# Optimization experiments

Hardware: AMD Instinct MI355X
Metric: run time of the kernel (lower is better)

## Reference

```python
import jax, jax.numpy as jnp
import numpy as np

N_BINS = 10
EPS = 1e-07


def setup_inputs() -> dict:
    key = jax.random.key(0)
    k1, k2 = jax.random.split(key)
    N, C = 8_000_000, 10
    logits = jax.random.uniform(k1, (N, C), dtype=jnp.float32)
    labels = jax.random.randint(k2, (N,), 0, C, dtype=jnp.int64)
    return {"logits": logits, "labels": labels}


def reference(logits, labels):
    # Faithful to torch forward: softmaxes = logits - 1e-7, then max/argmax over classes.
    boundaries = jnp.linspace(0.0, 1.0, N_BINS + 1, dtype=jnp.float32)
    sm = logits - EPS
    confidences = jnp.max(sm, axis=1)          # [N]
    predictions = jnp.argmax(sm, axis=1)       # [N]
    accuracies = (predictions == labels).astype(jnp.float32)

    # in_bin = conf > bin_lower & conf <= bin_upper  <=>  searchsorted(left) - 1
    # (boundaries[i-1] < conf <= boundaries[i] -> bin i-1)
    bin_idx = jnp.searchsorted(boundaries, confidences, side="left") - 1
    valid = (bin_idx >= 0) & (bin_idx < N_BINS)
    seg = jnp.where(valid, bin_idx, N_BINS)    # out-of-range -> overflow segment

    counts = jax.ops.segment_sum(jnp.ones_like(confidences), seg,
                                 num_segments=N_BINS + 1)[:N_BINS]
    correct = jax.ops.segment_sum(accuracies, seg,
                                  num_segments=N_BINS + 1)[:N_BINS]
    # accuracy_in_bin if prop_in_bin > 0 else 0
    return jnp.where(counts > 0, correct / jnp.maximum(counts, 1.0), 0.0)
```

## Files before the change

kernel.cpp:

```cpp
#include <hip/hip_runtime.h>

#define N_BINS 10
#define EPS 1e-7f

typedef unsigned int uint;


__global__ void zero_ws_kernel(uint* ws) {
    if (threadIdx.x < 2 * N_BINS) ws[threadIdx.x] = 0u;
}

__device__ __forceinline__ void process_row(const float v[10], int label,
                                            uint& c8, uint& k8, uint& c9, uint& k9,
                                            uint* scount, uint* scorrect) {
    float m = v[0] - EPS;
    int am = 0;
#pragma unroll
    for (int j = 1; j < 10; ++j) {
        float s = v[j] - EPS;
        if (s > m) { m = s; am = j; }
    }
    int acc = (am == label) ? 1 : 0;

    int idx = 0;
#pragma unroll
    for (int j = 0; j <= 10; ++j) {
        idx += ((0.1f * (float)j) < m) ? 1 : 0;
    }
    int bin = idx - 1;

    if (bin == 9)      { c9++; k9 += acc; }
    else if (bin == 8) { c8++; k8 += acc; }
    else if (bin >= 0 && bin < 8) {
        atomicAdd(&scount[bin], 1u);
        if (acc) atomicAdd(&scorrect[bin], 1u);
    }
}

__global__ void __launch_bounds__(512)
hist_kernel(const float* __restrict__ logits, const int* __restrict__ labels,
            uint* __restrict__ ws, int npairs, int n_rows) {
    __shared__ uint scount[N_BINS];
    __shared__ uint scorrect[N_BINS];
    if (threadIdx.x < N_BINS) { scount[threadIdx.x] = 0u; scorrect[threadIdx.x] = 0u; }
    __syncthreads();

    uint c8 = 0, k8 = 0, c9 = 0, k9 = 0;

    const int stride = gridDim.x * blockDim.x;
    const int tid0   = blockIdx.x * blockDim.x + threadIdx.x;

    for (int p = tid0; p < npairs; p += stride) {
        const float4* lp = reinterpret_cast<const float4*>(logits) + (size_t)p * 5;
        float4 q0 = lp[0], q1 = lp[1], q2 = lp[2], q3 = lp[3], q4 = lp[4];
        int2 lab = reinterpret_cast<const int2*>(labels)[p];

        float a[10] = { q0.x, q0.y, q0.z, q0.w, q1.x, q1.y, q1.z, q1.w, q2.x, q2.y };
        float b[10] = { q2.z, q2.w, q3.x, q3.y, q3.z, q3.w, q4.x, q4.y, q4.z, q4.w };

        process_row(a, lab.x, c8, k8, c9, k9, scount, scorrect);
        process_row(b, lab.y, c8, k8, c9, k9, scount, scorrect);
    }

    if ((n_rows & 1) && tid0 == 0) {
        const float* rp = logits + (size_t)(n_rows - 1) * 10;
        float t[10];
#pragma unroll
        for (int j = 0; j < 10; ++j) t[j] = rp[j];
        process_row(t, labels[n_rows - 1], c8, k8, c9, k9, scount, scorrect);
    }

#pragma unroll
    for (int off = 32; off > 0; off >>= 1) {
        c8 += __shfl_down(c8, off);
        k8 += __shfl_down(k8, off);
        c9 += __shfl_down(c9, off);
        k9 += __shfl_down(k9, off);
    }
    if ((threadIdx.x & 63) == 0) {
        atomicAdd(&scount[8], c8);
        atomicAdd(&scorrect[8], k8);
        atomicAdd(&scount[9], c9);
        atomicAdd(&scorrect[9], k9);
    }
    __syncthreads();

    if (threadIdx.x < N_BINS) {
        atomicAdd(&ws[threadIdx.x], scount[threadIdx.x]);
        atomicAdd(&ws[N_BINS + threadIdx.x], scorrect[threadIdx.x]);
    }
}

__global__ void finalize_kernel(const uint* __restrict__ ws, float* __restrict__ out) {
    if (threadIdx.x < N_BINS) {
        uint c = ws[threadIdx.x];
        uint k = ws[N_BINS + threadIdx.x];
        out[threadIdx.x] = (c > 0u) ? ((float)k / (float)c) : 0.0f;
    }
}

extern "C" void kernel_launch(void* const* d_in, const int* in_sizes, int n_in,
                              void* d_out, int out_size, void* d_ws, size_t ws_size,
                              hipStream_t stream) {
    const float* logits = (const float*)d_in[0];
    const int*   labels = (const int*)d_in[1];
    float*       out    = (float*)d_out;
    uint*        ws     = (uint*)d_ws;

    const int n_rows = in_sizes[1];
    const int npairs = n_rows / 2;

    zero_ws_kernel<<<1, 64, 0, stream>>>(ws);

    const int threads = 512;
    int blocks = (npairs + threads - 1) / threads;
    if (blocks > 1024) blocks = 1024;
    if (blocks < 1) blocks = 1;
    hist_kernel<<<blocks, threads, 0, stream>>>(logits, labels, ws, npairs, n_rows);

    finalize_kernel<<<1, 64, 0, stream>>>(ws, out);
}
```

Measured before the change: 441.2 us.

## Stage logits through LDS for fully coalesced global loads

Each block now loads a 256-pair chunk of logits with contiguous float4 loads spread across threads, writes it to shared memory, and then each thread reads its own 20 floats back from LDS. Before, each thread loaded 5 float4s at a stride of 80 bytes, so wave accesses were uncoalesced. The launch changes to 256 threads with up to 2048 blocks, and leftover pairs are handled by block 0. The cost is two barriers per chunk plus LDS traffic, with possible bank conflicts on the stride-5 float4 reads.

```diff
diff --git a/kernel.cpp b/kernel.cpp
--- a/kernel.cpp
+++ b/kernel.cpp
@@ -5,12 +5,16 @@
 
 typedef unsigned int uint;
 
+#define TPB 256
+#define PAIRS_PER_CHUNK 256
+#define CHUNK_F4 (PAIRS_PER_CHUNK * 5)
+
 
 __global__ void zero_ws_kernel(uint* ws) {
     if (threadIdx.x < 2 * N_BINS) ws[threadIdx.x] = 0u;
 }
 
-__device__ __forceinline__ void process_row(const float v[10], int label,
+__device__ __forceinline__ void process_row(const float* v, int label,
                                             uint& c8, uint& k8, uint& c9, uint& k9,
                                             uint* scount, uint* scorrect) {
     float m = v[0] - EPS;
@@ -37,9 +41,10 @@
     }
 }
 
-__global__ void __launch_bounds__(512)
+__global__ void __launch_bounds__(TPB)
 hist_kernel(const float* __restrict__ logits, const int* __restrict__ labels,
             uint* __restrict__ ws, int npairs, int n_rows) {
+    __shared__ float4 stage[CHUNK_F4];
     __shared__ uint scount[N_BINS];
     __shared__ uint scorrect[N_BINS];
     if (threadIdx.x < N_BINS) { scount[threadIdx.x] = 0u; scorrect[threadIdx.x] = 0u; }
@@ -47,27 +52,61 @@
 
     uint c8 = 0, k8 = 0, c9 = 0, k9 = 0;
 
-    const int stride = gridDim.x * blockDim.x;
-    const int tid0   = blockIdx.x * blockDim.x + threadIdx.x;
+    const int tid   = threadIdx.x;
+    const int nfull = npairs / PAIRS_PER_CHUNK;
+    const float4* gsrc = reinterpret_cast<const float4*>(logits);
+    const int2*   lsrc = reinterpret_cast<const int2*>(labels);
 
-    for (int p = tid0; p < npairs; p += stride) {
-        const float4* lp = reinterpret_cast<const float4*>(logits) + (size_t)p * 5;
-        float4 q0 = lp[0], q1 = lp[1], q2 = lp[2], q3 = lp[3], q4 = lp[4];
-        int2 lab = reinterpret_cast<const int2*>(labels)[p];
+    for (int c = blockIdx.x; c < nfull; c += gridDim.x) {
+        const size_t base = (size_t)c * CHUNK_F4;
 
-        float a[10] = { q0.x, q0.y, q0.z, q0.w, q1.x, q1.y, q1.z, q1.w, q2.x, q2.y };
-        float b[10] = { q2.z, q2.w, q3.x, q3.y, q3.z, q3.w, q4.x, q4.y, q4.z, q4.w };
+        float4 r0 = gsrc[base + tid];
+        float4 r1 = gsrc[base + tid + 1 * TPB];
+        float4 r2 = gsrc[base + tid + 2 * TPB];
+        float4 r3 = gsrc[base + tid + 3 * TPB];
+        float4 r4 = gsrc[base + tid + 4 * TPB];
+        int2 lab = lsrc[(size_t)c * PAIRS_PER_CHUNK + tid];
 
-        process_row(a, lab.x, c8, k8, c9, k9, scount, scorrect);
-        process_row(b, lab.y, c8, k8, c9, k9, scount, scorrect);
+        stage[tid]           = r0;
+        stage[tid + 1 * TPB] = r1;
+        stage[tid + 2 * TPB] = r2;
+        stage[tid + 3 * TPB] = r3;
+        stage[tid + 4 * TPB] = r4;
+        __syncthreads();
+
+        float4 a0 = stage[tid * 5 + 0];
+        float4 a1 = stage[tid * 5 + 1];
+        float4 a2 = stage[tid * 5 + 2];
+        float4 a3 = stage[tid * 5 + 3];
+        float4 a4 = stage[tid * 5 + 4];
+        float v[20] = { a0.x, a0.y, a0.z, a0.w, a1.x, a1.y, a1.z, a1.w,
+                        a2.x, a2.y, a2.z, a2.w, a3.x, a3.y, a3.z, a3.w,
+                        a4.x, a4.y, a4.z, a4.w };
+
+        process_row(v,      lab.x, c8, k8, c9, k9, scount, scorrect);
+        process_row(v + 10, lab.y, c8, k8, c9, k9, scount, scorrect);
+        __syncthreads();
     }
 
-    if ((n_rows & 1) && tid0 == 0) {
-        const float* rp = logits + (size_t)(n_rows - 1) * 10;
-        float t[10];
+    const int done_pairs = nfull * PAIRS_PER_CHUNK;
+    const int leftover   = npairs - done_pairs;
+    if (blockIdx.x == 0) {
+        if (tid < leftover) {
+            const float* rp = logits + (size_t)(done_pairs + tid) * 10;
+            float v[20];
 #pragma unroll
-        for (int j = 0; j < 10; ++j) t[j] = rp[j];
-        process_row(t, labels[n_rows - 1], c8, k8, c9, k9, scount, scorrect);
+            for (int j = 0; j < 20; ++j) v[j] = rp[j];
+            int2 lab = lsrc[done_pairs + tid];
+            process_row(v,      lab.x, c8, k8, c9, k9, scount, scorrect);
+            process_row(v + 10, lab.y, c8, k8, c9, k9, scount, scorrect);
+        }
+        if (tid == 0 && (n_rows & 1)) {
+            const float* rp = logits + (size_t)(n_rows - 1) * 10;
+            float t[10];
+#pragma unroll
+            for (int j = 0; j < 10; ++j) t[j] = rp[j];
+            process_row(t, labels[n_rows - 1], c8, k8, c9, k9, scount, scorrect);
+        }
     }
 
 #pragma unroll
@@ -112,11 +151,11 @@
 
     zero_ws_kernel<<<1, 64, 0, stream>>>(ws);
 
-    const int threads = 512;
-    int blocks = (npairs + threads - 1) / threads;
-    if (blocks > 1024) blocks = 1024;
-    if (blocks < 1) blocks = 1;
-    hist_kernel<<<blocks, threads, 0, stream>>>(logits, labels, ws, npairs, n_rows);
+    int blocks = 2048;
+    int nchunks = npairs / PAIRS_PER_CHUNK;
+    if (nchunks < 1) nchunks = 1;
+    if (blocks > nchunks) blocks = nchunks;
+    hist_kernel<<<blocks, TPB, 0, stream>>>(logits, labels, ws, npairs, n_rows);
 
     finalize_kernel<<<1, 64, 0, stream>>>(ws, out);
 }
```

Result: slower. 457.9 us (+3.8%).
